# Optimization experiments

Hardware: AMD Instinct MI355X
Metric: run time of the kernel (lower is better)

Reference implementation:

```python
import jax, jax.numpy as jnp
import numpy as np

N_NODES = 20000
N_INPUT = 64
K_MAX = 12
BITS = 64
N_OUT = 10
BATCH = 64
T = 128


def setup_inputs() -> dict:
    key = jax.random.key(0)
    ks = jax.random.split(key, 8)
    x = jax.random.randint(ks[0], (BATCH, T, BITS), 0, 2, dtype=jnp.int32)
    w_in = jax.random.randint(ks[1], (BITS, N_INPUT), 0, 2, dtype=jnp.int32)
    adj_list = jax.random.randint(ks[2], (N_NODES, K_MAX), 0, N_NODES, dtype=jnp.int32)
    adj_mask = jax.random.randint(ks[3], (N_NODES, K_MAX), 0, 2, dtype=jnp.int32)
    lut = jax.random.randint(ks[4], (N_NODES, 2 ** K_MAX), 0, 2, dtype=jnp.int32)
    init_states = jax.random.randint(ks[5], (1, N_NODES), 0, 2, dtype=jnp.int32)
    W_out = jax.random.normal(ks[6], (N_OUT, N_NODES - N_INPUT), dtype=jnp.float32) * 0.02
    b_out = jnp.zeros((N_OUT,), dtype=jnp.float32)
    return {"x": x, "w_in": w_in, "adj_list": adj_list, "adj_mask": adj_mask,
            "lut": lut, "init_states": init_states, "W_out": W_out, "b_out": b_out}


def reference(x, w_in, adj_list, adj_mask, lut, init_states, W_out, b_out):
    B, T_, bits = x.shape
    N, k = adj_list.shape
    I = w_in.shape[1]
    # powers_of_2, big-endian order as in make_minimal_powers_of_two (flip)
    powers = (2 ** jnp.arange(k - 1, -1, -1)).astype(jnp.int32)  # [k]
    no_neigh = ~(adj_mask.astype(bool).any(axis=1))              # [N] nodes w/o neighbours keep state
    node_ids = jnp.arange(N)
    states0 = jnp.broadcast_to(init_states, (B, N)).astype(jnp.int32)

    def step(states, x_t):
        # inject input: bipartite mapping of input bits onto first I nodes (OR-combine)
        u = ((x_t @ w_in) > 0).astype(jnp.int32)                 # [B, I]
        states = states.at[:, :I].set(u)
        # gather incoming neighbour states per node (irregular gather)
        neigh = jnp.take(states, adj_list, axis=1)               # [B, N, k]
        neigh = neigh * adj_mask[None, :, :]
        # bit-pack into LUT index
        idx = (neigh * powers[None, None, :]).sum(axis=-1)       # [B, N], < 2^k
        new = lut[node_ids[None, :], idx]                        # [B, N] LUT lookup
        new = jnp.where(no_neigh[None, :], states, new)
        return new, None

    states, _ = jax.lax.scan(step, states0, jnp.swapaxes(x, 0, 1))
    # readout on reservoir (non-input) nodes at final timestep
    feats = states[:, I:].astype(jnp.float32)                    # [B, N-I]
    out = jax.nn.sigmoid(feats @ W_out.T + b_out)                # [B, n_outputs]
    return out
```

## Files before the change

### kernel.cpp

```cpp
#include <hip/hip_runtime.h>
#include <cstdint>
#include <cstddef>


#define N_NODES   20000
#define N_INPUT   64
#define K_MAX     12
#define T_STEPS   128
#define N_BATCH   64
#define N_OUT     10
#define N_FEAT    (N_NODES - N_INPUT)
#define DUMMY_NODE 20000
#define ST_WORDS  20004

#define NBLK 512
#define NTHR 512
#define NPB  39
#define NPB_PAD 40
#define GO_OFF  512
#define GO_CNT  8
#define GO_STRIDE 32
#define FL_TOT  (GO_OFF + GO_CNT * GO_STRIDE)

#define RO_CHUNK 32
#define RO_NPC   623

typedef unsigned long long u64;

__global__ __launch_bounds__(256) void pack_x_kernel(const int* __restrict__ x,
                                                     u64* __restrict__ xp) {
  const int t = blockIdx.x;
  const int wave = threadIdx.x >> 6, lane = threadIdx.x & 63;
  for (int b = wave; b < N_BATCH; b += 4) {
    int v = x[((size_t)b * T_STEPS + t) * 64 + lane];
    u64 bal = __ballot(v != 0);
    if (lane == 0) xp[(size_t)t * N_BATCH + b] = bal;
  }
}

__global__ __launch_bounds__(256) void init_kernel(const int* __restrict__ inis,
                                                   const int* __restrict__ w_in,
                                                   const u64* __restrict__ xp,
                                                   u64* __restrict__ buf0,
                                                   u64* __restrict__ buf1,
                                                   u64* __restrict__ wcol,
                                                   unsigned* __restrict__ fl) {
  if (blockIdx.x < 79) {
    int n = blockIdx.x * 256 + threadIdx.x;
    if (n >= N_INPUT && n < ST_WORDS) {
      u64 w = (n < N_NODES && inis[n] != 0) ? ~0ull : 0ull;
      buf0[n] = w;
      buf1[n] = w;
    }
  } else {
    const int wave = threadIdx.x >> 6, lane = threadIdx.x & 63;
    u64 xw = xp[lane];
    for (int i = wave; i < 64; i += 4) {
      int wv = w_in[(size_t)lane * 64 + i];
      u64 wc = __ballot(wv != 0);
      if (lane == 0) wcol[i] = wc;
      u64 ub = __ballot((xw & wc) != 0);
      if (lane == 0) buf0[i] = ub;
    }
    for (int k = threadIdx.x; k < FL_TOT; k += 256)
      fl[k] = 0u;
  }
}

__global__ __launch_bounds__(64) void u_pre_kernel(const u64* __restrict__ xp,
                                                   const u64* __restrict__ wcol,
                                                   u64* __restrict__ u_all) {
  const int t = blockIdx.x, lane = threadIdx.x;
  u64 xw = xp[(size_t)t * N_BATCH + lane];
  for (int i = 0; i < 64; i++) {
    u64 ub = __ballot((xw & wcol[i]) != 0);
    if (lane == 0) u_all[(size_t)t * 64 + i] = ub;
  }
}

__device__ __forceinline__ u64 bit_transpose64(u64 w, int lane) {
  const u64 LO0 = 0x00000000FFFFFFFFull, LO1 = 0x0000FFFF0000FFFFull,
            LO2 = 0x00FF00FF00FF00FFull, LO3 = 0x0F0F0F0F0F0F0F0Full,
            LO4 = 0x3333333333333333ull, LO5 = 0x5555555555555555ull;
#define XP_STAGE(d, LO)                                                  \
  {                                                                      \
    u64 p = (u64)__shfl_xor((long long)w, (d), 64);                      \
    if (lane & (d)) w = ((p >> (d)) & (LO)) | (w & ~(LO));               \
    else            w = (w & (LO)) | ((p << (d)) & ~(LO));               \
  }
  XP_STAGE(32, LO0) XP_STAGE(16, LO1) XP_STAGE(8, LO2)
  XP_STAGE(4,  LO3) XP_STAGE(2,  LO4) XP_STAGE(1, LO5)
#undef XP_STAGE
  return w;
}

__global__ __launch_bounds__(NTHR, 4) void reservoir_kernel(
    const int* __restrict__ lut, const int* __restrict__ adj,
    const int* __restrict__ mask, const u64* __restrict__ u_all,
    u64* __restrict__ buf0, u64* __restrict__ buf1,
    unsigned* __restrict__ fl) {
  __shared__ u64 lut_lds[NPB_PAD * 64];
  __shared__ int adj_lds[NPB_PAD * K_MAX];
  __shared__ unsigned char hn_lds[NPB_PAD];

  const int bi = blockIdx.x;
  const int tid = threadIdx.x;
  const int wave = tid >> 6, lane = tid & 63;
  const int base = N_INPUT + bi * NPB;
  const int nloc = min(NPB, N_NODES - base);

  if (tid < NPB_PAD) {
    int i = tid, h = 0;
    if (i < nloc) {
      for (int j = 0; j < K_MAX; j++) {
        int m = mask[(size_t)(base + i) * K_MAX + j];
        int a = adj[(size_t)(base + i) * K_MAX + j];
        adj_lds[i * K_MAX + (K_MAX - 1 - j)] = m ? a : DUMMY_NODE;
        h |= m;
      }
    } else {
      for (int j = 0; j < K_MAX; j++) adj_lds[i * K_MAX + j] = DUMMY_NODE;
    }
    hn_lds[i] = (unsigned char)(h ? 1 : 0);
  }

  const int nwords = nloc * 64;
  const int* lp = lut + (size_t)base * 4096;
  for (int w0 = wave * 8; w0 < nwords; w0 += 64) {
    int v[8];
#pragma unroll
    for (int q = 0; q < 8; q++) {
      int widx = w0 + q;
      v[q] = (widx < nwords) ? lp[(size_t)widx * 64 + lane] : 0;
    }
#pragma unroll
    for (int q = 0; q < 8; q++) {
      int widx = w0 + q;
      u64 bal = __ballot(v[q] != 0);
      if (lane == 0 && widx < nwords) lut_lds[widx] = bal;
    }
  }
  __syncthreads();

  const int l0 = wave * 5;
  const int cnt = min(5, nloc - l0);

  int a0 = DUMMY_NODE;
  if (lane < 60) a0 = adj_lds[l0 * K_MAX + lane];
  unsigned hmask = 0;
#pragma unroll
  for (int i = 0; i < 5; i++) hmask |= (unsigned)hn_lds[l0 + i] << i;

  for (int t = 0; t < T_STEPS; t++) {
    u64* cur = (t & 1) ? buf1 : buf0;
    u64* nxt = (t & 1) ? buf0 : buf1;

    u64 w = __hip_atomic_load(&cur[a0], __ATOMIC_RELAXED, __HIP_MEMORY_SCOPE_AGENT);
    w = bit_transpose64(w, lane);

#pragma unroll
    for (int i = 0; i < 5; i++) {
      if (i < cnt) {
        unsigned idx = (unsigned)(w >> (12 * i)) & 0xFFFu;
        u64 g = lut_lds[(l0 + i) * 64 + (idx >> 6)];
        u64 res = __ballot((g >> (idx & 63)) & 1ull);
        if (lane == 0 && ((hmask >> i) & 1u))
          __hip_atomic_store(&nxt[base + l0 + i], res,
                             __ATOMIC_RELAXED, __HIP_MEMORY_SCOPE_AGENT);
      }
    }

    if (bi == NBLK - 1 && wave == 7 && t + 1 < T_STEPS) {
      u64 uw = u_all[(size_t)(t + 1) * 64 + lane];
      __hip_atomic_store(&nxt[lane], uw, __ATOMIC_RELAXED, __HIP_MEMORY_SCOPE_AGENT);
    }

    if (t != T_STEPS - 1) {
      const unsigned tgt = (unsigned)(t + 1);
      __syncthreads();
      __builtin_amdgcn_fence(__ATOMIC_RELEASE, "workgroup");
      if (tid == 0)
        __hip_atomic_store(&fl[bi], tgt, __ATOMIC_RELAXED, __HIP_MEMORY_SCOPE_AGENT);
      if (bi == 0 && wave == 0) {
        const u64* fp = (const u64*)fl;
        const u64 want = ((u64)tgt << 32) | (u64)tgt;
        for (;;) {
          u64 f0 = __hip_atomic_load(&fp[lane],       __ATOMIC_RELAXED, __HIP_MEMORY_SCOPE_AGENT);
          u64 f1 = __hip_atomic_load(&fp[64 + lane],  __ATOMIC_RELAXED, __HIP_MEMORY_SCOPE_AGENT);
          u64 f2 = __hip_atomic_load(&fp[128 + lane], __ATOMIC_RELAXED, __HIP_MEMORY_SCOPE_AGENT);
          u64 f3 = __hip_atomic_load(&fp[192 + lane], __ATOMIC_RELAXED, __HIP_MEMORY_SCOPE_AGENT);
          bool ok = (f0 == want) && (f1 == want) && (f2 == want) && (f3 == want);
          if (__all(ok)) break;
        }
        if (lane < GO_CNT)
          __hip_atomic_store(&fl[GO_OFF + lane * GO_STRIDE], tgt,
                             __ATOMIC_RELAXED, __HIP_MEMORY_SCOPE_AGENT);
      } else if (wave == 0) {
        unsigned* gp = &fl[GO_OFF + (bi & (GO_CNT - 1)) * GO_STRIDE];
        while (__hip_atomic_load(gp, __ATOMIC_RELAXED, __HIP_MEMORY_SCOPE_AGENT)
               < tgt) {  }
      }
      __builtin_amdgcn_fence(__ATOMIC_ACQUIRE, "workgroup");
      __syncthreads();
    }
  }
}

__global__ __launch_bounds__(256) void readout_part(const u64* __restrict__ st,
                                                    const float* __restrict__ Wout,
                                                    float* __restrict__ partial) {
  const int c = blockIdx.x / N_OUT;
  const int o = blockIdx.x % N_OUT;
  const int b = threadIdx.x & 63, k = threadIdx.x >> 6;
  const int n0 = c * RO_NPC, n1 = n0 + RO_NPC;
  float acc = 0.f;
  for (int n = n0 + k; n < n1; n += 4) {
    u64 s = st[N_INPUT + n];
    float w = Wout[(size_t)o * N_FEAT + n];
    acc += ((s >> b) & 1ull) ? w : 0.f;
  }
  __shared__ float red[4][64];
  red[k][b] = acc;
  __syncthreads();
  if (threadIdx.x < 64) {
    float tot = red[0][b] + red[1][b] + red[2][b] + red[3][b];
    partial[((size_t)c * N_OUT + o) * 64 + b] = tot;
  }
}

__global__ __launch_bounds__(640) void readout_final(const float* __restrict__ partial,
                                                     const float* __restrict__ bout,
                                                     float* __restrict__ out) {
  const int b = threadIdx.x & 63, o = threadIdx.x >> 6;
  float tot = bout[o];
  for (int c = 0; c < RO_CHUNK; c++)
    tot += partial[((size_t)c * N_OUT + o) * 64 + b];
  out[(size_t)b * N_OUT + o] = 1.f / (1.f + __expf(-tot));
}

extern "C" void kernel_launch(void* const* d_in, const int* in_sizes, int n_in,
                              void* d_out, int out_size, void* d_ws, size_t ws_size,
                              hipStream_t stream) {
  const int* x    = (const int*)d_in[0];
  const int* w_in = (const int*)d_in[1];
  const int* adj  = (const int*)d_in[2];
  const int* mask = (const int*)d_in[3];
  const int* lut  = (const int*)d_in[4];
  const int* inis = (const int*)d_in[5];
  const float* Wout = (const float*)d_in[6];
  const float* bout = (const float*)d_in[7];
  float* out = (float*)d_out;

  char* ws = (char*)d_ws;
  size_t off = 0;
  auto alloc = [&](size_t bytes) -> void* {
    void* p = ws + off;
    off += (bytes + 255) & ~(size_t)255;
    return p;
  };
  u64* buf0 = (u64*)alloc((size_t)ST_WORDS * 8);
  u64* buf1 = (u64*)alloc((size_t)ST_WORDS * 8);
  u64* xp   = (u64*)alloc((size_t)T_STEPS * N_BATCH * 8);
  u64* wcol = (u64*)alloc(64 * 8);
  u64* u_all = (u64*)alloc((size_t)T_STEPS * 64 * 8);
  unsigned* fl = (unsigned*)alloc((size_t)FL_TOT * 4);
  float* partial = (float*)alloc((size_t)RO_CHUNK * N_OUT * 64 * 4);
  (void)ws_size; (void)in_sizes; (void)n_in; (void)out_size;

  hipLaunchKernelGGL(pack_x_kernel, dim3(T_STEPS), dim3(256), 0, stream, x, xp);
  hipLaunchKernelGGL(init_kernel, dim3(80), dim3(256), 0, stream,
                     inis, w_in, xp, buf0, buf1, wcol, fl);
  hipLaunchKernelGGL(u_pre_kernel, dim3(T_STEPS), dim3(64), 0, stream,
                     xp, wcol, u_all);

  hipLaunchKernelGGL(reservoir_kernel, dim3(NBLK), dim3(NTHR), 0, stream,
                     lut, adj, mask, u_all, buf0, buf1, fl);

  hipLaunchKernelGGL(readout_part, dim3(RO_CHUNK * N_OUT), dim3(256), 0, stream,
                     buf0, Wout, partial);
  hipLaunchKernelGGL(readout_final, dim3(1), dim3(640), 0, stream,
                     partial, bout, out);
}
```

Measured before the change: 1.004 ms.

## Replace grid-wide barrier with tagged per-timestep state buffers for dataflow sync

Drops the per-timestep global flag barrier. Each timestep's state now lives in its own buffer, and every 64-bit word is paired with a copy XOR'd against a fixed key tag. Readers spin on their neighbour words until each pair checks out, so blocks wait only on the data they actually need. A new fill kernel prefills all 129 timestep buffers with invalid tags, or with constant valid values for nodes that never change. Input-node values are written ahead of time for every step. This trades a much larger workspace (about 41 MB written per call) and doubled load/store traffic for removing the global synchronisation latency on every step.

```diff
diff --git a/kernel.cpp b/kernel.cpp
--- a/kernel.cpp
+++ b/kernel.cpp
@@ -12,15 +12,14 @@
 #define N_FEAT    (N_NODES - N_INPUT)
 #define DUMMY_NODE 20000
 #define ST_WORDS  20004
+#define T_BUF     (T_STEPS + 1)
 
 #define NBLK 512
 #define NTHR 512
 #define NPB  39
 #define NPB_PAD 40
-#define GO_OFF  512
-#define GO_CNT  8
-#define GO_STRIDE 32
-#define FL_TOT  (GO_OFF + GO_CNT * GO_STRIDE)
+
+#define KTAG 0x9E3779B97F4A7C15ull
 
 #define RO_CHUNK 32
 #define RO_NPC   623
@@ -38,43 +37,49 @@
   }
 }
 
-__global__ __launch_bounds__(256) void init_kernel(const int* __restrict__ inis,
-                                                   const int* __restrict__ w_in,
-                                                   const u64* __restrict__ xp,
-                                                   u64* __restrict__ buf0,
-                                                   u64* __restrict__ buf1,
-                                                   u64* __restrict__ wcol,
-                                                   unsigned* __restrict__ fl) {
-  if (blockIdx.x < 79) {
-    int n = blockIdx.x * 256 + threadIdx.x;
-    if (n >= N_INPUT && n < ST_WORDS) {
-      u64 w = (n < N_NODES && inis[n] != 0) ? ~0ull : 0ull;
-      buf0[n] = w;
-      buf1[n] = w;
-    }
-  } else {
-    const int wave = threadIdx.x >> 6, lane = threadIdx.x & 63;
-    u64 xw = xp[lane];
-    for (int i = wave; i < 64; i += 4) {
-      int wv = w_in[(size_t)lane * 64 + i];
-      u64 wc = __ballot(wv != 0);
-      if (lane == 0) wcol[i] = wc;
-      u64 ub = __ballot((xw & wc) != 0);
-      if (lane == 0) buf0[i] = ub;
-    }
-    for (int k = threadIdx.x; k < FL_TOT; k += 256)
-      fl[k] = 0u;
+__global__ __launch_bounds__(256) void init_kernel(const int* __restrict__ w_in,
+                                                   u64* __restrict__ wcol) {
+  const int wave = threadIdx.x >> 6, lane = threadIdx.x & 63;
+  for (int i = wave; i < 64; i += 4) {
+    int wv = w_in[(size_t)lane * 64 + i];
+    u64 wc = __ballot(wv != 0);
+    if (lane == 0) wcol[i] = wc;
   }
 }
 
 __global__ __launch_bounds__(64) void u_pre_kernel(const u64* __restrict__ xp,
                                                    const u64* __restrict__ wcol,
-                                                   u64* __restrict__ u_all) {
+                                                   u64* __restrict__ st) {
   const int t = blockIdx.x, lane = threadIdx.x;
   u64 xw = xp[(size_t)t * N_BATCH + lane];
   for (int i = 0; i < 64; i++) {
     u64 ub = __ballot((xw & wcol[i]) != 0);
-    if (lane == 0) u_all[(size_t)t * 64 + i] = ub;
+    if (lane == 0) {
+      st[((size_t)t * ST_WORDS + i) * 2]     = ub;
+      st[((size_t)t * ST_WORDS + i) * 2 + 1] = ub ^ KTAG;
+    }
+  }
+}
+
+__global__ __launch_bounds__(512) void fill_kernel(const int* __restrict__ mask,
+                                                   const int* __restrict__ inis,
+                                                   u64* __restrict__ st) {
+  int n = N_INPUT + blockIdx.x * 512 + threadIdx.x;
+  if (n >= ST_WORDS) return;
+  bool hn = false; u64 iw = 0;
+  if (n < N_NODES) {
+    int h = 0;
+    for (int j = 0; j < K_MAX; j++) h |= mask[(size_t)n * K_MAX + j];
+    hn = (h != 0);
+    iw = inis[n] ? ~0ull : 0ull;
+  }
+  const u64 dt0 = iw,             gt0 = iw ^ KTAG;
+  const u64 dtr = hn ? 0ull : iw, gtr = hn ? ~KTAG : (iw ^ KTAG);
+  const int t0 = blockIdx.y * 4, t1 = min(t0 + 4, T_BUF);
+  for (int t = t0; t < t1; t++) {
+    u64 d = (t == 0) ? dt0 : dtr, g = (t == 0) ? gt0 : gtr;
+    st[((size_t)t * ST_WORDS + n) * 2]     = d;
+    st[((size_t)t * ST_WORDS + n) * 2 + 1] = g;
   }
 }
 
@@ -96,9 +101,7 @@
 
 __global__ __launch_bounds__(NTHR, 4) void reservoir_kernel(
     const int* __restrict__ lut, const int* __restrict__ adj,
-    const int* __restrict__ mask, const u64* __restrict__ u_all,
-    u64* __restrict__ buf0, u64* __restrict__ buf1,
-    unsigned* __restrict__ fl) {
+    const int* __restrict__ mask, u64* __restrict__ st) {
   __shared__ u64 lut_lds[NPB_PAD * 64];
   __shared__ int adj_lds[NPB_PAD * K_MAX];
   __shared__ unsigned char hn_lds[NPB_PAD];
@@ -152,61 +155,35 @@
   for (int i = 0; i < 5; i++) hmask |= (unsigned)hn_lds[l0 + i] << i;
 
   for (int t = 0; t < T_STEPS; t++) {
-    u64* cur = (t & 1) ? buf1 : buf0;
-    u64* nxt = (t & 1) ? buf0 : buf1;
-
-    u64 w = __hip_atomic_load(&cur[a0], __ATOMIC_RELAXED, __HIP_MEMORY_SCOPE_AGENT);
-    w = bit_transpose64(w, lane);
+    u64* stc = st + (size_t)t * ST_WORDS * 2;
+    u64* stn = st + (size_t)(t + 1) * ST_WORDS * 2;
+
+    u64 d = __hip_atomic_load(&stc[2 * a0],     __ATOMIC_RELAXED, __HIP_MEMORY_SCOPE_AGENT);
+    u64 g = __hip_atomic_load(&stc[2 * a0 + 1], __ATOMIC_RELAXED, __HIP_MEMORY_SCOPE_AGENT);
+    while (!__all((d ^ g) == KTAG)) {
+      d = __hip_atomic_load(&stc[2 * a0],     __ATOMIC_RELAXED, __HIP_MEMORY_SCOPE_AGENT);
+      g = __hip_atomic_load(&stc[2 * a0 + 1], __ATOMIC_RELAXED, __HIP_MEMORY_SCOPE_AGENT);
+    }
+    u64 w = bit_transpose64(d, lane);
 
 #pragma unroll
     for (int i = 0; i < 5; i++) {
       if (i < cnt) {
         unsigned idx = (unsigned)(w >> (12 * i)) & 0xFFFu;
-        u64 g = lut_lds[(l0 + i) * 64 + (idx >> 6)];
-        u64 res = __ballot((g >> (idx & 63)) & 1ull);
-        if (lane == 0 && ((hmask >> i) & 1u))
-          __hip_atomic_store(&nxt[base + l0 + i], res,
+        u64 gl = lut_lds[(l0 + i) * 64 + (idx >> 6)];
+        u64 res = __ballot((gl >> (idx & 63)) & 1ull);
+        if (lane == 0 && ((hmask >> i) & 1u)) {
+          __hip_atomic_store(&stn[2 * (base + l0 + i)], res,
                              __ATOMIC_RELAXED, __HIP_MEMORY_SCOPE_AGENT);
+          __hip_atomic_store(&stn[2 * (base + l0 + i) + 1], res ^ KTAG,
+                             __ATOMIC_RELAXED, __HIP_MEMORY_SCOPE_AGENT);
+        }
       }
     }
-
-    if (bi == NBLK - 1 && wave == 7 && t + 1 < T_STEPS) {
-      u64 uw = u_all[(size_t)(t + 1) * 64 + lane];
-      __hip_atomic_store(&nxt[lane], uw, __ATOMIC_RELAXED, __HIP_MEMORY_SCOPE_AGENT);
-    }
-
-    if (t != T_STEPS - 1) {
-      const unsigned tgt = (unsigned)(t + 1);
-      __syncthreads();
-      __builtin_amdgcn_fence(__ATOMIC_RELEASE, "workgroup");
-      if (tid == 0)
-        __hip_atomic_store(&fl[bi], tgt, __ATOMIC_RELAXED, __HIP_MEMORY_SCOPE_AGENT);
-      if (bi == 0 && wave == 0) {
-        const u64* fp = (const u64*)fl;
-        const u64 want = ((u64)tgt << 32) | (u64)tgt;
-        for (;;) {
-          u64 f0 = __hip_atomic_load(&fp[lane],       __ATOMIC_RELAXED, __HIP_MEMORY_SCOPE_AGENT);
-          u64 f1 = __hip_atomic_load(&fp[64 + lane],  __ATOMIC_RELAXED, __HIP_MEMORY_SCOPE_AGENT);
-          u64 f2 = __hip_atomic_load(&fp[128 + lane], __ATOMIC_RELAXED, __HIP_MEMORY_SCOPE_AGENT);
-          u64 f3 = __hip_atomic_load(&fp[192 + lane], __ATOMIC_RELAXED, __HIP_MEMORY_SCOPE_AGENT);
-          bool ok = (f0 == want) && (f1 == want) && (f2 == want) && (f3 == want);
-          if (__all(ok)) break;
-        }
-        if (lane < GO_CNT)
-          __hip_atomic_store(&fl[GO_OFF + lane * GO_STRIDE], tgt,
-                             __ATOMIC_RELAXED, __HIP_MEMORY_SCOPE_AGENT);
-      } else if (wave == 0) {
-        unsigned* gp = &fl[GO_OFF + (bi & (GO_CNT - 1)) * GO_STRIDE];
-        while (__hip_atomic_load(gp, __ATOMIC_RELAXED, __HIP_MEMORY_SCOPE_AGENT)
-               < tgt) {  }
-      }
-      __builtin_amdgcn_fence(__ATOMIC_ACQUIRE, "workgroup");
-      __syncthreads();
-    }
-  }
-}
-
-__global__ __launch_bounds__(256) void readout_part(const u64* __restrict__ st,
+  }
+}
+
+__global__ __launch_bounds__(256) void readout_part(const u64* __restrict__ st128,
                                                     const float* __restrict__ Wout,
                                                     float* __restrict__ partial) {
   const int c = blockIdx.x / N_OUT;
@@ -215,7 +192,7 @@
   const int n0 = c * RO_NPC, n1 = n0 + RO_NPC;
   float acc = 0.f;
   for (int n = n0 + k; n < n1; n += 4) {
-    u64 s = st[N_INPUT + n];
+    u64 s = st128[2 * (N_INPUT + n)];
     float w = Wout[(size_t)o * N_FEAT + n];
     acc += ((s >> b) & 1ull) ? w : 0.f;
   }
@@ -258,26 +235,24 @@
     off += (bytes + 255) & ~(size_t)255;
     return p;
   };
-  u64* buf0 = (u64*)alloc((size_t)ST_WORDS * 8);
-  u64* buf1 = (u64*)alloc((size_t)ST_WORDS * 8);
-  u64* xp   = (u64*)alloc((size_t)T_STEPS * N_BATCH * 8);
-  u64* wcol = (u64*)alloc(64 * 8);
-  u64* u_all = (u64*)alloc((size_t)T_STEPS * 64 * 8);
-  unsigned* fl = (unsigned*)alloc((size_t)FL_TOT * 4);
+  u64* st_all = (u64*)alloc((size_t)T_BUF * ST_WORDS * 16);
+  u64* xp     = (u64*)alloc((size_t)T_STEPS * N_BATCH * 8);
+  u64* wcol   = (u64*)alloc(64 * 8);
   float* partial = (float*)alloc((size_t)RO_CHUNK * N_OUT * 64 * 4);
   (void)ws_size; (void)in_sizes; (void)n_in; (void)out_size;
 
   hipLaunchKernelGGL(pack_x_kernel, dim3(T_STEPS), dim3(256), 0, stream, x, xp);
-  hipLaunchKernelGGL(init_kernel, dim3(80), dim3(256), 0, stream,
-                     inis, w_in, xp, buf0, buf1, wcol, fl);
+  hipLaunchKernelGGL(init_kernel, dim3(1), dim3(256), 0, stream, w_in, wcol);
+  hipLaunchKernelGGL(fill_kernel, dim3(39, 33), dim3(512), 0, stream,
+                     mask, inis, st_all);
   hipLaunchKernelGGL(u_pre_kernel, dim3(T_STEPS), dim3(64), 0, stream,
-                     xp, wcol, u_all);
+                     xp, wcol, st_all);
 
   hipLaunchKernelGGL(reservoir_kernel, dim3(NBLK), dim3(NTHR), 0, stream,
-                     lut, adj, mask, u_all, buf0, buf1, fl);
+                     lut, adj, mask, st_all);
 
   hipLaunchKernelGGL(readout_part, dim3(RO_CHUNK * N_OUT), dim3(256), 0, stream,
-                     buf0, Wout, partial);
+                     st_all + (size_t)T_STEPS * ST_WORDS * 2, Wout, partial);
   hipLaunchKernelGGL(readout_final, dim3(1), dim3(640), 0, stream,
                      partial, bout, out);
 }
```

Result: slower. 3.850 ms (+283.5%).
